# Performance work log

Hardware: AMD Instinct MI355X
Metric: run time of the kernel (lower is better)

The kernel has to match this reference:

```python
import jax, jax.numpy as jnp
import numpy as np

N = 12288      # users + phonePlacements + activities (4096 each)
S = 4096       # per-segment node count
M = 16384      # number of hyperedges
E = 393216     # incidences per branch
F = 256        # in/out channels for both conv layers
C = 128        # model_commonDim
SLOPE = 0.2    # all leaky slopes / negative_slope


def leaky(v, s=SLOPE):
    return jnp.where(v >= 0, v, s * v)


def hconv(h, hyperAttr, ni, ei, W, att, bias, hw):
    """PyG HypergraphConv, use_attention=True, heads=1, dropout=0 (eval)."""
    xl = h @ W                       # [N, F] node features through lin
    ea = hyperAttr @ W               # [M, F] hyperedge attrs through lin
    # attention logits per incidence, grouped-softmax over each node's incidences
    a = jnp.concatenate([xl[ni], ea[ei]], axis=-1) @ att   # [E]
    a = leaky(a, SLOPE)
    amax = jax.ops.segment_max(a, ni, num_segments=N)
    amax = jnp.where(jnp.isfinite(amax), amax, 0.0)
    ae = jnp.exp(a - amax[ni])
    asum = jax.ops.segment_sum(ae, ni, num_segments=N)
    alpha = ae / asum[ni]
    # degree normalizations
    D = jax.ops.segment_sum(hw[ei], ni, num_segments=N)
    Dinv = jnp.where(D > 0, 1.0 / D, 0.0)
    B = jax.ops.segment_sum(jnp.ones((E,), h.dtype), ei, num_segments=M)
    Binv = jnp.where(B > 0, 1.0 / B, 0.0)
    # node -> hyperedge, then hyperedge -> node (alpha applied in both)
    m = jax.ops.segment_sum((Binv[ei] * alpha)[:, None] * xl[ni], ei, num_segments=M)
    out = jax.ops.segment_sum((Dinv[ni] * alpha)[:, None] * m[ei], ni, num_segments=N)
    return out + bias


def setup_inputs() -> dict:
    key = jax.random.key(0)
    ks = jax.random.split(key, 32)
    d = {
        'g': jax.random.normal(ks[0], (N, F), jnp.float32),
        'x': jax.random.normal(ks[1], (4096, F), jnp.float32),
        'hyperWeight': jax.random.uniform(ks[2], (M,), jnp.float32),
        'hyperAttr': jax.random.normal(ks[3], (M, F), jnp.float32),
    }
    for i in range(3):
        d[f'ni{i}'] = jax.random.randint(ks[4 + i], (E,), 0, N).astype(jnp.int32)
        d[f'ei{i}'] = jax.random.randint(ks[7 + i], (E,), 0, M).astype(jnp.int32)
    s = 0.05
    d['W0'] = jax.random.normal(ks[10], (3, F, F), jnp.float32) * s
    d['b0'] = jnp.zeros((3, F), jnp.float32)
    d['Wh1'] = jax.random.normal(ks[11], (3, F, F), jnp.float32) * s
    d['att1'] = jax.random.normal(ks[12], (3, 2 * F), jnp.float32) * s
    d['bc1'] = jnp.zeros((3, F), jnp.float32)
    d['W1'] = jax.random.normal(ks[13], (3, F, F), jnp.float32) * s
    d['b1'] = jnp.zeros((3, F), jnp.float32)
    d['Wh2'] = jax.random.normal(ks[14], (3, F, F), jnp.float32) * s
    d['att2'] = jax.random.normal(ks[15], (3, 2 * F), jnp.float32) * s
    d['bc2'] = jnp.zeros((3, F), jnp.float32)
    d['Wg'] = jax.random.normal(ks[16], (3, F, C), jnp.float32) * s
    d['bg'] = jnp.zeros((3, C), jnp.float32)
    d['Wx'] = jax.random.normal(ks[17], (3, F, C), jnp.float32) * s
    d['bx'] = jnp.zeros((3, C), jnp.float32)
    return d


def reference(g, x, hyperWeight, hyperAttr, ni0, ei0, ni1, ei1, ni2, ei2,
              W0, b0, Wh1, att1, bc1, W1, b1, Wh2, att2, bc2, Wg, bg, Wx, bx):
    nis, eis = (ni0, ni1, ni2), (ei0, ei1, ei2)
    # layer0: per-segment Linear, cat, LeakyReLU
    h = jnp.concatenate([g[i * S:(i + 1) * S] @ W0[i] + b0[i] for i in range(3)], axis=0)
    h = leaky(h)
    # hyper1: 3 conv branches summed, then act1 (dropout=0)
    h = sum(hconv(h, hyperAttr, nis[k], eis[k], Wh1[k], att1[k], bc1[k], hyperWeight)
            for k in range(3))
    h = leaky(h)
    # layer1: per-segment Linear, cat, LeakyReLU
    h = jnp.concatenate([h[i * S:(i + 1) * S] @ W1[i] + b1[i] for i in range(3)], axis=0)
    h = leaky(h)
    # hyper2
    h = sum(hconv(h, hyperAttr, nis[k], eis[k], Wh2[k], att2[k], bc2[k], hyperWeight)
            for k in range(3))
    h = leaky(h)
    # projections to common space
    new_g = [leaky(h[i * S:(i + 1) * S] @ Wg[i] + bg[i]) for i in range(3)]
    xs = [leaky(x @ Wx[i] + bx[i]) for i in range(3)]
    result = jnp.concatenate([xs[1] @ new_g[1].T, xs[2] @ new_g[2].T], axis=1)
    return result, h
```

## Files before the change

### kernel.cpp

```cpp
#include <hip/hip_runtime.h>
#include <cmath>

#define E_INC   393216
#define NN_     12288
#define MM_     16384
#define FDIM    256
#define CDIM    128

#define BM 64
#define BN 64
#define BK 16

__host__ __device__ inline int cntBase(int r){ return r<3 ? r*NN_ : 3*NN_ + (r-3)*MM_; }
__host__ __device__ inline int stBase(int r){ return r<3 ? r*(NN_+1) : 3*(NN_+1) + (r-3)*(MM_+1); }

__device__ __forceinline__ float lrelu(float v){ return v >= 0.0f ? v : 0.2f*v; }

struct Ptrs6 { const int* p[6]; };

__global__ __launch_bounds__(256) void hist_kernel(Ptrs6 ip, int* __restrict__ cnt){
  int r = blockIdx.y;
  int e = blockIdx.x*256 + threadIdx.x;
  atomicAdd(&cnt[cntBase(r) + ip.p[r][e]], 1);
}

__global__ __launch_bounds__(1024) void scan_kernel(const int* __restrict__ cnt,
                                                    int* __restrict__ starts,
                                                    int* __restrict__ cur){
  int r = blockIdx.x;
  int nb = (r<3) ? NN_ : MM_;
  int cb = cntBase(r), sb = stBase(r);
  int t = threadIdx.x;
  int chunk = nb >> 10;
  int o = t*chunk;
  int s = 0;
  for (int j=0;j<chunk;++j) s += cnt[cb+o+j];
  __shared__ int sd[1024];
  sd[t] = s; __syncthreads();
  for (int ofs=1; ofs<1024; ofs<<=1){
    int v = (t>=ofs) ? sd[t-ofs] : 0;
    __syncthreads();
    sd[t] += v; __syncthreads();
  }
  int run = sd[t] - s;
  for (int j=0;j<chunk;++j){
    int c = cnt[cb+o+j];
    starts[sb+o+j] = run; cur[cb+o+j] = run;
    run += c;
  }
  if (t == 1023) starts[sb+nb] = run;
}

__global__ __launch_bounds__(256) void fill_kernel(Ptrs6 ip, int* __restrict__ cur,
                                                   int* __restrict__ lists){
  int r = blockIdx.y;
  int e = blockIdx.x*256 + threadIdx.x;
  int key = ip.p[r][e];
  int pos = atomicAdd(&cur[cntBase(r)+key], 1);
  lists[(size_t)r*E_INC + pos] = e;
}

__global__ __launch_bounds__(256) void sortb_kernel(const int* __restrict__ starts,
                                                    int* __restrict__ lists){
  int r = blockIdx.y;
  int nb = (r<3) ? NN_ : MM_;
  int wid = (blockIdx.x*256 + threadIdx.x) >> 6;
  int lane = threadIdx.x & 63;
  if (wid >= nb) return;
  int sb = stBase(r);
  int lo = starts[sb+wid], hi = starts[sb+wid+1];
  int len = hi - lo;
  if (len <= 1) return;
  int* lst = lists + (size_t)r*E_INC;
  if (len <= 64){
    int v = (lane < len) ? lst[lo+lane] : 0x7fffffff;
#pragma unroll
    for (int k = 2; k <= 64; k <<= 1){
#pragma unroll
      for (int j = k>>1; j > 0; j >>= 1){
        int o = __shfl_xor(v, j);
        bool up    = ((lane & k) == 0);
        bool lower = ((lane & j) == 0);
        int mn = min(v,o), mx = max(v,o);
        v = (lower == up) ? mn : mx;
      }
    }
    if (lane < len) lst[lo+lane] = v;
  } else if (lane == 0) {
    for (int i=lo+1; i<hi; ++i){
      int key = lst[i]; int j = i-1;
      while (j>=lo && lst[j]>key){ lst[j+1]=lst[j]; --j; }
      lst[j+1]=key;
    }
  }
}

#define FMA4(i, a) \
  acc[i][0]=fmaf(a,bv.x,acc[i][0]); acc[i][1]=fmaf(a,bv.y,acc[i][1]); \
  acc[i][2]=fmaf(a,bv.z,acc[i][2]); acc[i][3]=fmaf(a,bv.w,acc[i][3]);

__global__ __launch_bounds__(256)
void gemm_nn(const float* __restrict__ A, const float* __restrict__ W,
             const float* __restrict__ bias, float* __restrict__ C,
             int N, int segShift, int act)
{
  __shared__ alignas(16) float As[BK][BM+4];
  __shared__ alignas(16) float Bs[BK][BN+4];
  int t = threadIdx.x;
  int bm = blockIdx.x * BM;
  int bn = blockIdx.y * BN;
  int seg = bm >> segShift;
  const float* Wp = W + (size_t)seg * FDIM * N;
  int tx = t & 15, ty = t >> 4;
  int arow = t >> 2, akq = (t & 3) << 2;
  int brow = t >> 4, bcg = (t & 15) << 2;

  float acc[4][4] = {};
  for (int k0 = 0; k0 < FDIM; k0 += BK){
    float4 a4 = *(const float4*)(A + (size_t)(bm+arow)*FDIM + k0 + akq);
    As[akq+0][arow]=a4.x; As[akq+1][arow]=a4.y; As[akq+2][arow]=a4.z; As[akq+3][arow]=a4.w;
    float4 b4 = *(const float4*)(Wp + (size_t)(k0+brow)*N + bn + bcg);
    *(float4*)&Bs[brow][bcg] = b4;
    __syncthreads();
#pragma unroll
    for (int kk=0; kk<BK; ++kk){
      float4 av = *(const float4*)&As[kk][ty<<2];
      float4 bv = *(const float4*)&Bs[kk][tx<<2];
      FMA4(0, av.x) FMA4(1, av.y) FMA4(2, av.z) FMA4(3, av.w)
    }
    __syncthreads();
  }
  int c0 = bn + (tx<<2);
  float4 bb = make_float4(0.f,0.f,0.f,0.f);
  if (bias) bb = *(const float4*)(bias + (size_t)seg*N + c0);
#pragma unroll
  for (int i=0;i<4;++i){
    float4 o = make_float4(acc[i][0],acc[i][1],acc[i][2],acc[i][3]);
    if (bias){ o.x+=bb.x; o.y+=bb.y; o.z+=bb.z; o.w+=bb.w; }
    if (act){ o.x=lrelu(o.x); o.y=lrelu(o.y); o.z=lrelu(o.z); o.w=lrelu(o.w); }
    *(float4*)(C + (size_t)(bm+(ty<<2)+i)*N + c0) = o;
  }
}

__global__ __launch_bounds__(256)
void gemm_nt(const float* __restrict__ A, const float* __restrict__ B,
             float* __restrict__ C, int ldc, int colOff)
{
  __shared__ alignas(16) float As[BK][BM+4];
  __shared__ alignas(16) float Bs[BK][BN+4];
  int t = threadIdx.x;
  int bm = blockIdx.x * BM;
  int bn = blockIdx.y * BN;
  int tx = t & 15, ty = t >> 4;
  int arow = t >> 2, akq = (t & 3) << 2;

  float acc[4][4] = {};
  for (int k0 = 0; k0 < CDIM; k0 += BK){
    float4 a4 = *(const float4*)(A + (size_t)(bm+arow)*CDIM + k0 + akq);
    As[akq+0][arow]=a4.x; As[akq+1][arow]=a4.y; As[akq+2][arow]=a4.z; As[akq+3][arow]=a4.w;
    float4 b4 = *(const float4*)(B + (size_t)(bn+arow)*CDIM + k0 + akq);
    Bs[akq+0][arow]=b4.x; Bs[akq+1][arow]=b4.y; Bs[akq+2][arow]=b4.z; Bs[akq+3][arow]=b4.w;
    __syncthreads();
#pragma unroll
    for (int kk=0; kk<BK; ++kk){
      float4 av = *(const float4*)&As[kk][ty<<2];
      float4 bv = *(const float4*)&Bs[kk][tx<<2];
      FMA4(0, av.x) FMA4(1, av.y) FMA4(2, av.z) FMA4(3, av.w)
    }
    __syncthreads();
  }
#pragma unroll
  for (int i=0;i<4;++i){
    float4 o = make_float4(acc[i][0],acc[i][1],acc[i][2],acc[i][3]);
    *(float4*)(C + (size_t)(bm+(ty<<2)+i)*ldc + colOff + bn + (tx<<2)) = o;
  }
}

__global__ __launch_bounds__(256)
void rowdot(const float* __restrict__ Mx, const float* __restrict__ vec,
            float* __restrict__ out, int rows)
{
  int g = blockIdx.x*256 + threadIdx.x;
  int w = g >> 6, lane = g & 63;
  if (w >= rows) return;
  const float* r = Mx + (size_t)w*FDIM;
  double s = 0.0;
#pragma unroll
  for (int c=lane; c<FDIM; c+=64) s = fma((double)r[c], (double)vec[c], s);
  for (int ofs=32; ofs; ofs>>=1) s += __shfl_down(s, ofs);
  if (lane==0) out[w] = (float)s;
}

__global__ __launch_bounds__(256)
void node_stats(const int* __restrict__ starts, const int* __restrict__ list,
                const int* __restrict__ ei, const float* __restrict__ s1,
                const float* __restrict__ s2, const float* __restrict__ hw,
                float* __restrict__ amax, float* __restrict__ asum,
                float* __restrict__ dinv)
{
  int g = blockIdx.x*256 + threadIdx.x;
  int w = g >> 6, lane = g & 63;
  if (w >= NN_) return;
  int lo = starts[w], hi = starts[w+1];
  float s1n = s1[w];
  float mx = -INFINITY;
  for (int i=lo+lane; i<hi; i+=64){
    int e = list[i];
    mx = fmaxf(mx, lrelu(s1n + s2[ei[e]]));
  }
  for (int ofs=32; ofs; ofs>>=1) mx = fmaxf(mx, __shfl_xor(mx, ofs));
  if (lo == hi) mx = 0.0f;
  double se = 0.0, sd = 0.0;
  for (int i=lo+lane; i<hi; i+=64){
    int e = list[i]; int m = ei[e];
    float a = lrelu(s1n + s2[m]);
    se += (double)expf(a - mx);
    sd += (double)hw[m];
  }
  for (int ofs=32; ofs; ofs>>=1){ se += __shfl_xor(se, ofs); sd += __shfl_xor(sd, ofs); }
  if (lane==0){
    amax[w] = mx;
    asum[w] = (float)se;
    float D = (float)sd;
    dinv[w] = (D > 0.0f) ? 1.0f/D : 0.0f;
  }
}

__global__ __launch_bounds__(256)
void alpha_kernel(const int* __restrict__ ni, const int* __restrict__ ei,
                  const float* __restrict__ s1, const float* __restrict__ s2,
                  const float* __restrict__ amax, const float* __restrict__ asum,
                  float* __restrict__ alpha)
{
  int e = blockIdx.x*256 + threadIdx.x;
  int n = ni[e];
  float a = lrelu(s1[n] + s2[ei[e]]);
  alpha[e] = expf(a - amax[n]) / asum[n];
}

__global__ __launch_bounds__(256)
void m_kernel(const int* __restrict__ estarts, const int* __restrict__ elist,
              const int* __restrict__ ni, const float* __restrict__ alpha,
              const float* __restrict__ xl, float* __restrict__ m)
{
  int g = blockIdx.x*256 + threadIdx.x;
  int w = g >> 6, lane = g & 63;
  if (w >= MM_) return;
  int lo = estarts[w], hi = estarts[w+1];
  float binv = (hi > lo) ? 1.0f/(float)(hi-lo) : 0.0f;
  float ax=0.f, ay=0.f, az=0.f, aw=0.f;
  int col = lane << 2;
  for (int i=lo; i<hi; ++i){
    int e = elist[i];
    float c = __fmul_rn(binv, alpha[e]);
    const float4 x4 = *(const float4*)(xl + (size_t)ni[e]*FDIM + col);
    ax = __fadd_rn(ax, __fmul_rn(c, x4.x));
    ay = __fadd_rn(ay, __fmul_rn(c, x4.y));
    az = __fadd_rn(az, __fmul_rn(c, x4.z));
    aw = __fadd_rn(aw, __fmul_rn(c, x4.w));
  }
  *(float4*)(m + (size_t)w*FDIM + col) = make_float4(ax,ay,az,aw);
}

__global__ __launch_bounds__(256)
void out_kernel(const int* __restrict__ nstarts, const int* __restrict__ nlist,
                const int* __restrict__ ei, const float* __restrict__ alpha,
                const float* __restrict__ dinv, const float* __restrict__ m,
                const float* __restrict__ bias, float* __restrict__ accb,
                int first, int finalAct)
{
  int g = blockIdx.x*256 + threadIdx.x;
  int w = g >> 6, lane = g & 63;
  if (w >= NN_) return;
  int lo = nstarts[w], hi = nstarts[w+1];
  float dv = dinv[w];
  float ax=0.f, ay=0.f, az=0.f, aw=0.f;
  int col = lane << 2;
  for (int i=lo; i<hi; ++i){
    int e = nlist[i];
    float c = __fmul_rn(dv, alpha[e]);
    const float4 m4 = *(const float4*)(m + (size_t)ei[e]*FDIM + col);
    ax = __fadd_rn(ax, __fmul_rn(c, m4.x));
    ay = __fadd_rn(ay, __fmul_rn(c, m4.y));
    az = __fadd_rn(az, __fmul_rn(c, m4.z));
    aw = __fadd_rn(aw, __fmul_rn(c, m4.w));
  }
  const float4 b4 = *(const float4*)(bias + col);
  ax = __fadd_rn(ax, b4.x); ay = __fadd_rn(ay, b4.y);
  az = __fadd_rn(az, b4.z); aw = __fadd_rn(aw, b4.w);
  float* p = accb + (size_t)w*FDIM + col;
  if (!first){
    float4 pr = *(const float4*)p;
    ax = __fadd_rn(pr.x, ax); ay = __fadd_rn(pr.y, ay);
    az = __fadd_rn(pr.z, az); aw = __fadd_rn(pr.w, aw);
  }
  if (finalAct){ ax=lrelu(ax); ay=lrelu(ay); az=lrelu(az); aw=lrelu(aw); }
  *(float4*)p = make_float4(ax,ay,az,aw);
}

extern "C" void kernel_launch(void* const* d_in, const int* in_sizes, int n_in,
                              void* d_out, int out_size, void* d_ws, size_t ws_size,
                              hipStream_t stream)
{
  (void)in_sizes; (void)n_in; (void)out_size; (void)ws_size;
  const float* g     = (const float*)d_in[0];
  const float* x     = (const float*)d_in[1];
  const float* hw    = (const float*)d_in[2];
  const float* hattr = (const float*)d_in[3];
  const int* ni[3]   = {(const int*)d_in[4], (const int*)d_in[6], (const int*)d_in[8]};
  const int* ei[3]   = {(const int*)d_in[5], (const int*)d_in[7], (const int*)d_in[9]};
  const float* W0  = (const float*)d_in[10];
  const float* b0  = (const float*)d_in[11];
  const float* Wh1 = (const float*)d_in[12];
  const float* att1= (const float*)d_in[13];
  const float* bc1 = (const float*)d_in[14];
  const float* W1  = (const float*)d_in[15];
  const float* b1  = (const float*)d_in[16];
  const float* Wh2 = (const float*)d_in[17];
  const float* att2= (const float*)d_in[18];
  const float* bc2 = (const float*)d_in[19];
  const float* Wg  = (const float*)d_in[20];
  const float* bg  = (const float*)d_in[21];
  const float* Wx  = (const float*)d_in[22];
  const float* bx  = (const float*)d_in[23];
  float* outp = (float*)d_out;

  char* base = (char*)d_ws;
  size_t off = 0;
  auto alloc = [&](size_t bytes)->void*{
    void* p = base + off;
    off = (off + bytes + 255) & ~(size_t)255;
    return p;
  };
  const size_t SZ_H = (size_t)NN_*FDIM;
  float* hA    = (float*)alloc(SZ_H*4);
  float* xl    = (float*)alloc(SZ_H*4);
  float* acc   = (float*)alloc(SZ_H*4);
  float* mbuf  = (float*)alloc((size_t)MM_*FDIM*4);
  float* alphab= (float*)alloc((size_t)E_INC*4);
  float* s1    = (float*)alloc(NN_*4);
  float* s2    = (float*)alloc(MM_*4);
  float* vv    = (float*)alloc(FDIM*4);
  float* amax  = (float*)alloc(NN_*4);
  float* asum  = (float*)alloc(NN_*4);
  float* dinvb = (float*)alloc(NN_*4);
  float* ng1   = (float*)alloc((size_t)4096*CDIM*4);
  float* ng2   = (float*)alloc((size_t)4096*CDIM*4);
  float* xs1   = (float*)alloc((size_t)4096*CDIM*4);
  float* xs2   = (float*)alloc((size_t)4096*CDIM*4);
  int*   cnt   = (int*)alloc((size_t)(3*NN_+3*MM_)*4);
  int*   cur   = (int*)alloc((size_t)(3*NN_+3*MM_)*4);
  int*   stb   = (int*)alloc((size_t)(3*(NN_+1)+3*(MM_+1))*4);
  int*   lists = (int*)alloc((size_t)6*E_INC*4);

  hipMemsetAsync(cnt, 0, (size_t)(3*NN_+3*MM_)*4, stream);
  Ptrs6 ip{{ni[0],ni[1],ni[2],ei[0],ei[1],ei[2]}};
  hist_kernel <<<dim3(E_INC/256,6),256,0,stream>>>(ip, cnt);
  scan_kernel <<<6,1024,0,stream>>>(cnt, stb, cur);
  fill_kernel <<<dim3(E_INC/256,6),256,0,stream>>>(ip, cur, lists);
  sortb_kernel<<<dim3(4096,6),256,0,stream>>>(stb, lists);

  gemm_nn<<<dim3(192,4),256,0,stream>>>(g, W0, b0, hA, FDIM, 12, 1);

  auto hyper = [&](const float* hin, const float* Whs, const float* atts, const float* bcs){
    for (int k=0;k<3;++k){
      const float* Wk   = Whs + (size_t)k*FDIM*FDIM;
      const float* attA = atts + (size_t)k*2*FDIM;
      const float* attB = attA + FDIM;
      const int* nst = stb + stBase(k);
      const int* nls = lists + (size_t)k*E_INC;
      const int* est = stb + stBase(3+k);
      const int* els = lists + (size_t)(3+k)*E_INC;
      gemm_nn    <<<dim3(192,4),256,0,stream>>>(hin, Wk, nullptr, xl, FDIM, 30, 0);
      rowdot     <<<64,  256,0,stream>>>(Wk, attB, vv, FDIM);
      rowdot     <<<3072,256,0,stream>>>(xl, attA, s1, NN_);
      rowdot     <<<4096,256,0,stream>>>(hattr, vv, s2, MM_);
      node_stats <<<3072,256,0,stream>>>(nst, nls, ei[k], s1, s2, hw, amax, asum, dinvb);
      alpha_kernel<<<E_INC/256,256,0,stream>>>(ni[k], ei[k], s1, s2, amax, asum, alphab);
      m_kernel   <<<4096,256,0,stream>>>(est, els, ni[k], alphab, xl, mbuf);
      out_kernel <<<3072,256,0,stream>>>(nst, nls, ei[k], alphab, dinvb, mbuf,
                                         bcs + (size_t)k*FDIM, acc, k==0, k==2);
    }
  };

  hyper(hA, Wh1, att1, bc1);
  gemm_nn<<<dim3(192,4),256,0,stream>>>(acc, W1, b1, hA, FDIM, 12, 1);
  hyper(hA, Wh2, att2, bc2);

  gemm_nn<<<dim3(64,2),256,0,stream>>>(acc + (size_t)1*4096*FDIM, Wg + (size_t)1*FDIM*CDIM,
                                       bg + 1*CDIM, ng1, CDIM, 30, 1);
  gemm_nn<<<dim3(64,2),256,0,stream>>>(acc + (size_t)2*4096*FDIM, Wg + (size_t)2*FDIM*CDIM,
                                       bg + 2*CDIM, ng2, CDIM, 30, 1);
  gemm_nn<<<dim3(64,2),256,0,stream>>>(x, Wx + (size_t)1*FDIM*CDIM, bx + 1*CDIM, xs1, CDIM, 30, 1);
  gemm_nn<<<dim3(64,2),256,0,stream>>>(x, Wx + (size_t)2*FDIM*CDIM, bx + 2*CDIM, xs2, CDIM, 30, 1);

  gemm_nt<<<dim3(64,64),256,0,stream>>>(xs1, ng1, outp, 8192, 0);
  gemm_nt<<<dim3(64,64),256,0,stream>>>(xs2, ng2, outp, 8192, 4096);

  hipMemcpyAsync(outp + (size_t)4096*8192, acc, SZ_H*4, hipMemcpyDeviceToDevice, stream);
}
```

Measured before the change: 1.961 ms.

## Replace global-atomic CSR build with two-level partitioned sort; enlarge GEMM register tiles

The CSR incidence-list build no longer does a global-atomic histogram and fill over all keys. It first scatters incidences into 128-key coarse partitions using block-local shared-memory histograms, then sorts each partition by fine key in shared memory. This cuts contention on global atomics and scattered writes. Separately, gemm_nn moves to 128x64 tiles with 8x4 per-thread outputs and gemm_nt to 128x128 tiles with 8x8, to raise arithmetic intensity at the cost of fewer blocks and more registers. The partition buffer reuses mbuf.

```diff
diff --git a/kernel.cpp b/kernel.cpp
--- a/kernel.cpp
+++ b/kernel.cpp
@@ -6,58 +6,119 @@
 #define MM_     16384
 #define FDIM    256
 #define CDIM    128
-
-#define BM 64
-#define BN 64
-#define BK 16
-
-__host__ __device__ inline int cntBase(int r){ return r<3 ? r*NN_ : 3*NN_ + (r-3)*MM_; }
+#define PKEYS   128
+#define LCAP    6144
+
 __host__ __device__ inline int stBase(int r){ return r<3 ? r*(NN_+1) : 3*(NN_+1) + (r-3)*(MM_+1); }
+__host__ __device__ inline int nParts(int r){ return (r<3 ? NN_ : MM_) / PKEYS; }
 
 __device__ __forceinline__ float lrelu(float v){ return v >= 0.0f ? v : 0.2f*v; }
 
 struct Ptrs6 { const int* p[6]; };
 
-__global__ __launch_bounds__(256) void hist_kernel(Ptrs6 ip, int* __restrict__ cnt){
-  int r = blockIdx.y;
-  int e = blockIdx.x*256 + threadIdx.x;
-  atomicAdd(&cnt[cntBase(r) + ip.p[r][e]], 1);
-}
-
-__global__ __launch_bounds__(1024) void scan_kernel(const int* __restrict__ cnt,
-                                                    int* __restrict__ starts,
-                                                    int* __restrict__ cur){
-  int r = blockIdx.x;
-  int nb = (r<3) ? NN_ : MM_;
-  int cb = cntBase(r), sb = stBase(r);
-  int t = threadIdx.x;
-  int chunk = nb >> 10;
-  int o = t*chunk;
-  int s = 0;
-  for (int j=0;j<chunk;++j) s += cnt[cb+o+j];
-  __shared__ int sd[1024];
-  sd[t] = s; __syncthreads();
-  for (int ofs=1; ofs<1024; ofs<<=1){
+__global__ __launch_bounds__(256) void coarse_hist(Ptrs6 keys, int* __restrict__ ccnt){
+  __shared__ int h[PKEYS];
+  int r = blockIdx.y, t = threadIdx.x;
+  if (t < PKEYS) h[t] = 0;
+  __syncthreads();
+  int base = blockIdx.x * 4096;
+  const int* ka = keys.p[r];
+  for (int j=0;j<16;++j) atomicAdd(&h[ka[base + j*256 + t] >> 7], 1);
+  __syncthreads();
+  if (t < PKEYS) atomicAdd(&ccnt[r*PKEYS + t], h[t]);
+}
+
+__global__ __launch_bounds__(128) void coarse_scan(const int* __restrict__ ccnt,
+                                                   int* __restrict__ cstart,
+                                                   int* __restrict__ ccur){
+  int r = blockIdx.x, t = threadIdx.x;
+  int P = nParts(r);
+  int c = (t < P) ? ccnt[r*PKEYS + t] : 0;
+  __shared__ int sd[128];
+  sd[t] = c; __syncthreads();
+  for (int ofs=1; ofs<128; ofs<<=1){
     int v = (t>=ofs) ? sd[t-ofs] : 0;
-    __syncthreads();
-    sd[t] += v; __syncthreads();
-  }
-  int run = sd[t] - s;
-  for (int j=0;j<chunk;++j){
-    int c = cnt[cb+o+j];
-    starts[sb+o+j] = run; cur[cb+o+j] = run;
-    run += c;
-  }
-  if (t == 1023) starts[sb+nb] = run;
-}
-
-__global__ __launch_bounds__(256) void fill_kernel(Ptrs6 ip, int* __restrict__ cur,
-                                                   int* __restrict__ lists){
-  int r = blockIdx.y;
-  int e = blockIdx.x*256 + threadIdx.x;
-  int key = ip.p[r][e];
-  int pos = atomicAdd(&cur[cntBase(r)+key], 1);
-  lists[(size_t)r*E_INC + pos] = e;
+    __syncthreads(); sd[t] += v; __syncthreads();
+  }
+  int excl = sd[t] - c;
+  cstart[r*129 + t] = excl;
+  ccur[r*PKEYS + t] = excl;
+  if (t == 127) cstart[r*129 + 128] = sd[127];
+}
+
+__global__ __launch_bounds__(256) void part_scatter(Ptrs6 keys, int* __restrict__ ccur,
+                                                    int* __restrict__ pbuf){
+  __shared__ int h[PKEYS];
+  __shared__ int cur[PKEYS];
+  int r = blockIdx.y, t = threadIdx.x;
+  if (t < PKEYS) h[t] = 0;
+  __syncthreads();
+  int base = blockIdx.x * 4096;
+  const int* ka = keys.p[r];
+  int myk[16];
+  for (int j=0;j<16;++j){
+    myk[j] = ka[base + j*256 + t] >> 7;
+    atomicAdd(&h[myk[j]], 1);
+  }
+  __syncthreads();
+  if (t < PKEYS) cur[t] = atomicAdd(&ccur[r*PKEYS + t], h[t]);
+  __syncthreads();
+  int* pb = pbuf + (size_t)r * E_INC;
+  for (int j=0;j<16;++j){
+    int pos = atomicAdd(&cur[myk[j]], 1);
+    pb[pos] = base + j*256 + t;
+  }
+}
+
+__global__ __launch_bounds__(256) void fine_build(Ptrs6 keys, const int* __restrict__ cstart,
+                                                  const int* __restrict__ pbuf,
+                                                  int* __restrict__ starts,
+                                                  int* __restrict__ lists){
+  __shared__ unsigned short kb[LCAP];
+  __shared__ int ob[LCAP];
+  __shared__ int h[PKEYS], ls[PKEYS], lc[PKEYS];
+  int r = blockIdx.y, p = blockIdx.x, t = threadIdx.x;
+  int P = nParts(r);
+  if (p >= P) return;
+  int lo = cstart[r*129 + p], hi = cstart[r*129 + p + 1];
+  int len = hi - lo;
+  if (t < PKEYS) h[t] = 0;
+  __syncthreads();
+  const int* ka = keys.p[r];
+  const int* pb = pbuf + (size_t)r * E_INC;
+  int* lst = lists + (size_t)r * E_INC;
+  int kbase = p << 7;
+  int sb = stBase(r);
+  if (len <= LCAP){
+    for (int i=t; i<len; i+=256){
+      int e = pb[lo+i];
+      int k = ka[e] - kbase;
+      kb[i] = (unsigned short)k;
+      atomicAdd(&h[k], 1);
+    }
+    __syncthreads();
+    if (t == 0){ int run = 0; for (int k=0;k<PKEYS;++k){ ls[k]=run; lc[k]=run; run+=h[k]; } }
+    __syncthreads();
+    for (int i=t; i<len; i+=256){
+      int pos = atomicAdd(&lc[kb[i]], 1);
+      ob[pos] = pb[lo+i];
+    }
+    __syncthreads();
+    for (int i=t; i<len; i+=256) lst[lo+i] = ob[i];
+    if (t < PKEYS) starts[sb + kbase + t] = lo + ls[t];
+  } else {
+    for (int i=t; i<len; i+=256) atomicAdd(&h[ka[pb[lo+i]] - kbase], 1);
+    __syncthreads();
+    if (t == 0){ int run = 0; for (int k=0;k<PKEYS;++k){ ls[k]=run; lc[k]=run; run+=h[k]; } }
+    __syncthreads();
+    for (int i=t; i<len; i+=256){
+      int e = pb[lo+i];
+      int pos = atomicAdd(&lc[ka[e] - kbase], 1);
+      lst[lo+pos] = e;
+    }
+    if (t < PKEYS) starts[sb + kbase + t] = lo + ls[t];
+  }
+  if (p == P-1 && t == 0) starts[sb + (r<3 ? NN_ : MM_)] = hi;
 }
 
 __global__ __launch_bounds__(256) void sortb_kernel(const int* __restrict__ starts,
@@ -95,38 +156,42 @@
   }
 }
 
-#define FMA4(i, a) \
-  acc[i][0]=fmaf(a,bv.x,acc[i][0]); acc[i][1]=fmaf(a,bv.y,acc[i][1]); \
-  acc[i][2]=fmaf(a,bv.z,acc[i][2]); acc[i][3]=fmaf(a,bv.w,acc[i][3]);
-
 __global__ __launch_bounds__(256)
 void gemm_nn(const float* __restrict__ A, const float* __restrict__ W,
              const float* __restrict__ bias, float* __restrict__ C,
              int N, int segShift, int act)
 {
-  __shared__ alignas(16) float As[BK][BM+4];
-  __shared__ alignas(16) float Bs[BK][BN+4];
+  __shared__ alignas(16) float As[16][132];
+  __shared__ alignas(16) float Bs[16][68];
   int t = threadIdx.x;
-  int bm = blockIdx.x * BM;
-  int bn = blockIdx.y * BN;
+  int bm = blockIdx.x * 128;
+  int bn = blockIdx.y * 64;
   int seg = bm >> segShift;
   const float* Wp = W + (size_t)seg * FDIM * N;
   int tx = t & 15, ty = t >> 4;
-  int arow = t >> 2, akq = (t & 3) << 2;
-  int brow = t >> 4, bcg = (t & 15) << 2;
-
-  float acc[4][4] = {};
-  for (int k0 = 0; k0 < FDIM; k0 += BK){
-    float4 a4 = *(const float4*)(A + (size_t)(bm+arow)*FDIM + k0 + akq);
-    As[akq+0][arow]=a4.x; As[akq+1][arow]=a4.y; As[akq+2][arow]=a4.z; As[akq+3][arow]=a4.w;
-    float4 b4 = *(const float4*)(Wp + (size_t)(k0+brow)*N + bn + bcg);
-    *(float4*)&Bs[brow][bcg] = b4;
-    __syncthreads();
-#pragma unroll
-    for (int kk=0; kk<BK; ++kk){
-      float4 av = *(const float4*)&As[kk][ty<<2];
+  int arow = t >> 1, akq = (t & 1) << 3;
+  int brow = t >> 4, bcol = (t & 15) << 2;
+
+  float acc[8][4] = {};
+  for (int k0 = 0; k0 < FDIM; k0 += 16){
+    const float* ap = A + (size_t)(bm+arow)*FDIM + k0 + akq;
+    float4 a0 = *(const float4*)(ap);
+    float4 a1 = *(const float4*)(ap + 4);
+    As[akq+0][arow]=a0.x; As[akq+1][arow]=a0.y; As[akq+2][arow]=a0.z; As[akq+3][arow]=a0.w;
+    As[akq+4][arow]=a1.x; As[akq+5][arow]=a1.y; As[akq+6][arow]=a1.z; As[akq+7][arow]=a1.w;
+    *(float4*)&Bs[brow][bcol] = *(const float4*)(Wp + (size_t)(k0+brow)*N + bn + bcol);
+    __syncthreads();
+#pragma unroll
+    for (int kk=0; kk<16; ++kk){
+      float4 x0 = *(const float4*)&As[kk][ty<<3];
+      float4 x1 = *(const float4*)&As[kk][(ty<<3)+4];
       float4 bv = *(const float4*)&Bs[kk][tx<<2];
-      FMA4(0, av.x) FMA4(1, av.y) FMA4(2, av.z) FMA4(3, av.w)
+      float af[8] = {x0.x,x0.y,x0.z,x0.w,x1.x,x1.y,x1.z,x1.w};
+      float bf[4] = {bv.x,bv.y,bv.z,bv.w};
+#pragma unroll
+      for (int i=0;i<8;++i)
+#pragma unroll
+        for (int j=0;j<4;++j) acc[i][j] = fmaf(af[i], bf[j], acc[i][j]);
     }
     __syncthreads();
   }
@@ -134,11 +199,11 @@
   float4 bb = make_float4(0.f,0.f,0.f,0.f);
   if (bias) bb = *(const float4*)(bias + (size_t)seg*N + c0);
 #pragma unroll
-  for (int i=0;i<4;++i){
+  for (int i=0;i<8;++i){
     float4 o = make_float4(acc[i][0],acc[i][1],acc[i][2],acc[i][3]);
     if (bias){ o.x+=bb.x; o.y+=bb.y; o.z+=bb.z; o.w+=bb.w; }
     if (act){ o.x=lrelu(o.x); o.y=lrelu(o.y); o.z=lrelu(o.z); o.w=lrelu(o.w); }
-    *(float4*)(C + (size_t)(bm+(ty<<2)+i)*N + c0) = o;
+    *(float4*)(C + (size_t)(bm+(ty<<3)+i)*N + c0) = o;
   }
 }
 
@@ -146,33 +211,48 @@
 void gemm_nt(const float* __restrict__ A, const float* __restrict__ B,
              float* __restrict__ C, int ldc, int colOff)
 {
-  __shared__ alignas(16) float As[BK][BM+4];
-  __shared__ alignas(16) float Bs[BK][BN+4];
+  __shared__ alignas(16) float As[16][132];
+  __shared__ alignas(16) float Bs[16][132];
   int t = threadIdx.x;
-  int bm = blockIdx.x * BM;
-  int bn = blockIdx.y * BN;
+  int bm = blockIdx.x * 128;
+  int bn = blockIdx.y * 128;
   int tx = t & 15, ty = t >> 4;
-  int arow = t >> 2, akq = (t & 3) << 2;
-
-  float acc[4][4] = {};
-  for (int k0 = 0; k0 < CDIM; k0 += BK){
-    float4 a4 = *(const float4*)(A + (size_t)(bm+arow)*CDIM + k0 + akq);
-    As[akq+0][arow]=a4.x; As[akq+1][arow]=a4.y; As[akq+2][arow]=a4.z; As[akq+3][arow]=a4.w;
-    float4 b4 = *(const float4*)(B + (size_t)(bn+arow)*CDIM + k0 + akq);
-    Bs[akq+0][arow]=b4.x; Bs[akq+1][arow]=b4.y; Bs[akq+2][arow]=b4.z; Bs[akq+3][arow]=b4.w;
-    __syncthreads();
-#pragma unroll
-    for (int kk=0; kk<BK; ++kk){
-      float4 av = *(const float4*)&As[kk][ty<<2];
-      float4 bv = *(const float4*)&Bs[kk][tx<<2];
-      FMA4(0, av.x) FMA4(1, av.y) FMA4(2, av.z) FMA4(3, av.w)
-    }
-    __syncthreads();
-  }
-#pragma unroll
-  for (int i=0;i<4;++i){
-    float4 o = make_float4(acc[i][0],acc[i][1],acc[i][2],acc[i][3]);
-    *(float4*)(C + (size_t)(bm+(ty<<2)+i)*ldc + colOff + bn + (tx<<2)) = o;
+  int arow = t >> 1, akq = (t & 1) << 3;
+
+  float acc[8][8] = {};
+  for (int k0 = 0; k0 < CDIM; k0 += 16){
+    const float* ap = A + (size_t)(bm+arow)*CDIM + k0 + akq;
+    float4 a0 = *(const float4*)(ap);
+    float4 a1 = *(const float4*)(ap + 4);
+    As[akq+0][arow]=a0.x; As[akq+1][arow]=a0.y; As[akq+2][arow]=a0.z; As[akq+3][arow]=a0.w;
+    As[akq+4][arow]=a1.x; As[akq+5][arow]=a1.y; As[akq+6][arow]=a1.z; As[akq+7][arow]=a1.w;
+    const float* bp = B + (size_t)(bn+arow)*CDIM + k0 + akq;
+    float4 b0 = *(const float4*)(bp);
+    float4 b1 = *(const float4*)(bp + 4);
+    Bs[akq+0][arow]=b0.x; Bs[akq+1][arow]=b0.y; Bs[akq+2][arow]=b0.z; Bs[akq+3][arow]=b0.w;
+    Bs[akq+4][arow]=b1.x; Bs[akq+5][arow]=b1.y; Bs[akq+6][arow]=b1.z; Bs[akq+7][arow]=b1.w;
+    __syncthreads();
+#pragma unroll
+    for (int kk=0; kk<16; ++kk){
+      float4 x0 = *(const float4*)&As[kk][ty<<3];
+      float4 x1 = *(const float4*)&As[kk][(ty<<3)+4];
+      float4 y0 = *(const float4*)&Bs[kk][tx<<3];
+      float4 y1 = *(const float4*)&Bs[kk][(tx<<3)+4];
+      float af[8] = {x0.x,x0.y,x0.z,x0.w,x1.x,x1.y,x1.z,x1.w};
+      float bf[8] = {y0.x,y0.y,y0.z,y0.w,y1.x,y1.y,y1.z,y1.w};
+#pragma unroll
+      for (int i=0;i<8;++i)
+#pragma unroll
+        for (int j=0;j<8;++j) acc[i][j] = fmaf(af[i], bf[j], acc[i][j]);
+    }
+    __syncthreads();
+  }
+  int c0 = colOff + bn + (tx<<3);
+#pragma unroll
+  for (int i=0;i<8;++i){
+    float* cp = C + (size_t)(bm+(ty<<3)+i)*ldc + c0;
+    *(float4*)(cp)   = make_float4(acc[i][0],acc[i][1],acc[i][2],acc[i][3]);
+    *(float4*)(cp+4) = make_float4(acc[i][4],acc[i][5],acc[i][6],acc[i][7]);
   }
 }
 
@@ -348,19 +428,22 @@
   float* ng2   = (float*)alloc((size_t)4096*CDIM*4);
   float* xs1   = (float*)alloc((size_t)4096*CDIM*4);
   float* xs2   = (float*)alloc((size_t)4096*CDIM*4);
-  int*   cnt   = (int*)alloc((size_t)(3*NN_+3*MM_)*4);
-  int*   cur   = (int*)alloc((size_t)(3*NN_+3*MM_)*4);
+  int*   ccnt  = (int*)alloc((size_t)6*PKEYS*4);
+  int*   ccur  = (int*)alloc((size_t)6*PKEYS*4);
+  int*   cstart= (int*)alloc((size_t)6*129*4);
   int*   stb   = (int*)alloc((size_t)(3*(NN_+1)+3*(MM_+1))*4);
   int*   lists = (int*)alloc((size_t)6*E_INC*4);
-
-  hipMemsetAsync(cnt, 0, (size_t)(3*NN_+3*MM_)*4, stream);
+  int*   pbuf  = (int*)mbuf;
+
+  hipMemsetAsync(ccnt, 0, (size_t)6*PKEYS*4, stream);
   Ptrs6 ip{{ni[0],ni[1],ni[2],ei[0],ei[1],ei[2]}};
-  hist_kernel <<<dim3(E_INC/256,6),256,0,stream>>>(ip, cnt);
-  scan_kernel <<<6,1024,0,stream>>>(cnt, stb, cur);
-  fill_kernel <<<dim3(E_INC/256,6),256,0,stream>>>(ip, cur, lists);
+  coarse_hist <<<dim3(96,6),256,0,stream>>>(ip, ccnt);
+  coarse_scan <<<6,128,0,stream>>>(ccnt, cstart, ccur);
+  part_scatter<<<dim3(96,6),256,0,stream>>>(ip, ccur, pbuf);
+  fine_build  <<<dim3(128,6),256,0,stream>>>(ip, cstart, pbuf, stb, lists);
   sortb_kernel<<<dim3(4096,6),256,0,stream>>>(stb, lists);
 
-  gemm_nn<<<dim3(192,4),256,0,stream>>>(g, W0, b0, hA, FDIM, 12, 1);
+  gemm_nn<<<dim3(96,4),256,0,stream>>>(g, W0, b0, hA, FDIM, 12, 1);
 
   auto hyper = [&](const float* hin, const float* Whs, const float* atts, const float* bcs){
     for (int k=0;k<3;++k){
@@ -371,7 +454,7 @@
       const int* nls = lists + (size_t)k*E_INC;
       const int* est = stb + stBase(3+k);
       const int* els = lists + (size_t)(3+k)*E_INC;
-      gemm_nn    <<<dim3(192,4),256,0,stream>>>(hin, Wk, nullptr, xl, FDIM, 30, 0);
+      gemm_nn    <<<dim3(96,4),256,0,stream>>>(hin, Wk, nullptr, xl, FDIM, 30, 0);
       rowdot     <<<64,  256,0,stream>>>(Wk, attB, vv, FDIM);
       rowdot     <<<3072,256,0,stream>>>(xl, attA, s1, NN_);
       rowdot     <<<4096,256,0,stream>>>(hattr, vv, s2, MM_);
@@ -384,18 +467,18 @@
   };
 
   hyper(hA, Wh1, att1, bc1);
-  gemm_nn<<<dim3(192,4),256,0,stream>>>(acc, W1, b1, hA, FDIM, 12, 1);
+  gemm_nn<<<dim3(96,4),256,0,stream>>>(acc, W1, b1, hA, FDIM, 12, 1);
   hyper(hA, Wh2, att2, bc2);
 
-  gemm_nn<<<dim3(64,2),256,0,stream>>>(acc + (size_t)1*4096*FDIM, Wg + (size_t)1*FDIM*CDIM,
+  gemm_nn<<<dim3(32,2),256,0,stream>>>(acc + (size_t)1*4096*FDIM, Wg + (size_t)1*FDIM*CDIM,
                                        bg + 1*CDIM, ng1, CDIM, 30, 1);
-  gemm_nn<<<dim3(64,2),256,0,stream>>>(acc + (size_t)2*4096*FDIM, Wg + (size_t)2*FDIM*CDIM,
+  gemm_nn<<<dim3(32,2),256,0,stream>>>(acc + (size_t)2*4096*FDIM, Wg + (size_t)2*FDIM*CDIM,
                                        bg + 2*CDIM, ng2, CDIM, 30, 1);
-  gemm_nn<<<dim3(64,2),256,0,stream>>>(x, Wx + (size_t)1*FDIM*CDIM, bx + 1*CDIM, xs1, CDIM, 30, 1);
-  gemm_nn<<<dim3(64,2),256,0,stream>>>(x, Wx + (size_t)2*FDIM*CDIM, bx + 2*CDIM, xs2, CDIM, 30, 1);
-
-  gemm_nt<<<dim3(64,64),256,0,stream>>>(xs1, ng1, outp, 8192, 0);
-  gemm_nt<<<dim3(64,64),256,0,stream>>>(xs2, ng2, outp, 8192, 4096);
+  gemm_nn<<<dim3(32,2),256,0,stream>>>(x, Wx + (size_t)1*FDIM*CDIM, bx + 1*CDIM, xs1, CDIM, 30, 1);
+  gemm_nn<<<dim3(32,2),256,0,stream>>>(x, Wx + (size_t)2*FDIM*CDIM, bx + 2*CDIM, xs2, CDIM, 30, 1);
+
+  gemm_nt<<<dim3(32,32),256,0,stream>>>(xs1, ng1, outp, 8192, 0);
+  gemm_nt<<<dim3(32,32),256,0,stream>>>(xs2, ng2, outp, 8192, 4096);
 
   hipMemcpyAsync(outp + (size_t)4096*8192, acc, SZ_H*4, hipMemcpyDeviceToDevice, stream);
 }
```

Measured after the change: 1.829 ms. 6.7% less time.
